# Kernel optimization log

Measured on AMD Instinct MI355X. Metric: run time of the kernel, lower is better.

The kernel has to match this reference:

```python
import jax, jax.numpy as jnp
import numpy as np

TOPK = 2


def setup_inputs() -> dict:
    key = jax.random.key(0)
    k1, k2, k3, k4, k5 = jax.random.split(key, 5)
    D, H, E = 1024, 1408, 8
    hidden_states = jax.random.normal(k1, (2, 1024, D), dtype=jnp.float32)
    gate_w = jax.random.normal(k2, (E, D), dtype=jnp.float32) * 0.02
    w1g = jax.random.normal(k3, (E, D, H), dtype=jnp.float32) * 0.02
    w1u = jax.random.normal(k4, (E, D, H), dtype=jnp.float32) * 0.02
    w2 = jax.random.normal(k5, (E, H, D), dtype=jnp.float32) * 0.02
    return {"hidden_states": hidden_states, "gate_w": gate_w, "w1g": w1g, "w1u": w1u, "w2": w2}


def reference(hidden_states, gate_w, w1g, w1u, w2):
    # hidden_states: [B, S, D]; expert weights: w1g/w1u [E, D, H], w2 [E, H, D]
    B, S, D = hidden_states.shape
    E = gate_w.shape[0]
    x = hidden_states.reshape(-1, D)  # [T, D]
    T = x.shape[0]

    # --- MoEGate: softmax scores, top-k routing (no topk renorm) ---
    logits = x @ gate_w.T                      # [T, E]
    scores = jax.nn.softmax(logits, axis=-1)   # [T, E]
    topk_w, topk_idx = jax.lax.top_k(scores, TOPK)  # [T, K]

    # Per-token combine coefficient for each expert: coeff[t, e] = sum_k w[t,k] * (idx[t,k]==e)
    coeff = jnp.zeros((T, E), dtype=x.dtype).at[jnp.arange(T)[:, None], topk_idx].add(topk_w)

    # --- Grouped expert MLP (swiglu): identical math to permute + grouped GEMM + unpermute ---
    g = jnp.einsum('td,edh->teh', x, w1g)      # [T, E, H]
    u = jnp.einsum('td,edh->teh', x, w1u)      # [T, E, H]
    h = jax.nn.silu(g) * u                     # [T, E, H]
    y = jnp.einsum('teh,te,ehd->td', h, coeff, w2)  # [T, D]
    return y.reshape(B, S, D)
```

## Files before the change

kernel.cpp:

```cpp
#include <hip/hip_runtime.h>

#define TOK 2048
#define DDIM 1024
#define HDIM 1408
#define ENUM 8
#define NSLOT (2 * TOK)
#define UP_NB 22
#define UP_KS 32
#define DN_NB 16
#define DN_KS 44

typedef unsigned int uint;
typedef unsigned short ushort;

using bf16x8 = __attribute__((ext_vector_type(8))) __bf16;
using f32x4  = __attribute__((ext_vector_type(4))) float;

__device__ __forceinline__ float silu_f(float g) {
    return g / (1.0f + __expf(-g));
}

__device__ __forceinline__ ushort cvt_bf16(float f) {
    uint u = __float_as_uint(f);
    u += 0x7FFFu + ((u >> 16) & 1u);
    return (ushort)(u >> 16);
}

__device__ __forceinline__ void gl2lds16(const void* g, void* l) {
    __builtin_amdgcn_global_load_lds(
        (const __attribute__((address_space(1))) uint*)g,
        (__attribute__((address_space(3))) uint*)l, 16, 0, 0);
}

__global__ __launch_bounds__(64) void gate_kernel(
    const float* __restrict__ x, const float* __restrict__ gw,
    int* __restrict__ counts, int* __restrict__ toks,
    float* __restrict__ wslot, ushort* __restrict__ xb)
{
    const int t = blockIdx.x;
    const int lane = threadIdx.x;
    const float* xr = x + (size_t)t * DDIM;
    ushort* xbr = xb + (size_t)t * DDIM;
    float xv[16];
#pragma unroll
    for (int i = 0; i < 16; ++i) xv[i] = xr[lane + 64 * i];
#pragma unroll
    for (int i = 0; i < 16; ++i) xbr[lane + 64 * i] = cvt_bf16(xv[i]);
    float logit[ENUM];
#pragma unroll
    for (int e = 0; e < ENUM; ++e) {
        const float* gr = gw + (size_t)e * DDIM;
        float acc = 0.f;
#pragma unroll
        for (int i = 0; i < 16; ++i) acc += xv[i] * gr[lane + 64 * i];
#pragma unroll
        for (int s = 32; s > 0; s >>= 1) acc += __shfl_xor(acc, s, 64);
        logit[e] = acc;
    }
    if (lane == 0) {
        float mx = logit[0];
#pragma unroll
        for (int e = 1; e < ENUM; ++e) mx = fmaxf(mx, logit[e]);
        float p[ENUM]; float se = 0.f;
#pragma unroll
        for (int e = 0; e < ENUM; ++e) { p[e] = __expf(logit[e] - mx); se += p[e]; }
        float inv = 1.0f / se;
#pragma unroll
        for (int e = 0; e < ENUM; ++e) p[e] *= inv;
        int i0 = 0;
#pragma unroll
        for (int e = 1; e < ENUM; ++e) if (p[e] > p[i0]) i0 = e;
        int i1 = (i0 == 0) ? 1 : 0;
#pragma unroll
        for (int e = 0; e < ENUM; ++e) if (e != i0 && p[e] > p[i1]) i1 = e;
        int pos0 = atomicAdd(&counts[i0], 1);
        toks[i0 * TOK + pos0] = (t << 1);
        wslot[(t << 1)] = p[i0];
        int pos1 = atomicAdd(&counts[i1], 1);
        toks[i1 * TOK + pos1] = (t << 1) | 1;
        wslot[(t << 1) | 1] = p[i1];
    }
}

__device__ __forceinline__ void tcast64_body(
    const float* __restrict__ src, ushort* __restrict__ dst, int N, int KS, int NB,
    int e, int ks, int nb, int tid)
{
    __shared__ float Ls[32][68];
    const float* st = src + (size_t)e * ((size_t)KS * 32) * N + (size_t)(ks * 32) * N + nb * 64;
    const int n4 = (tid & 15) * 4;
#pragma unroll
    for (int r = 0; r < 2; ++r) {
        int k = (tid >> 4) + r * 16;
        float4 v = *(const float4*)(st + (size_t)k * N + n4);
        Ls[k][n4 + 0] = v.x; Ls[k][n4 + 1] = v.y; Ls[k][n4 + 2] = v.z; Ls[k][n4 + 3] = v.w;
    }
    __syncthreads();

    ushort* dt = dst + ((((size_t)e * NB + nb) * KS) + ks) * 2048;
    const int nn = tid >> 2;
    const int kk0 = (tid & 3) * 8;
    ushort o[8];
#pragma unroll
    for (int j = 0; j < 8; ++j) o[j] = cvt_bf16(Ls[kk0 + j][nn]);
    *(uint4*)(dt + nn * 32 + kk0) = *(uint4*)o;
}

__global__ __launch_bounds__(256) void tcast_w1_kernel(
    const float* __restrict__ w1g, const float* __restrict__ w1u,
    ushort* __restrict__ BgP, ushort* __restrict__ BuP)
{
    const int z = blockIdx.z;
    const float* src = (z & 8) ? w1u : w1g;
    ushort* dst = (z & 8) ? BuP : BgP;
    tcast64_body(src, dst, HDIM, UP_KS, UP_NB, z & 7, blockIdx.x, blockIdx.y, threadIdx.x);
}

__global__ __launch_bounds__(256) void tcast_w2_kernel(
    const float* __restrict__ w2, ushort* __restrict__ W2P)
{
    tcast64_body(w2, W2P, DDIM, DN_KS, DN_NB, blockIdx.z, blockIdx.x, blockIdx.y, threadIdx.x);
}

__global__ __launch_bounds__(256, 4) void up_mfma(
    const ushort* __restrict__ xb, const ushort* __restrict__ BgP,
    const ushort* __restrict__ BuP, const int* __restrict__ counts,
    const int* __restrict__ toks, ushort* __restrict__ Hbuf)
{
    const int e = blockIdx.z;
    const int cnt = counts[e];
    const int m0 = blockIdx.y * 64;
    if (m0 >= cnt) return;
    const int nb = blockIdx.x;
    const int tid = threadIdx.x;
    const int w = tid >> 6;
    const int lane = tid & 63;
    const int q = lane >> 4;
    const int l15 = lane & 15;
    const int wr = w >> 1;
    const int wc = w & 1;

    __shared__ ushort As[2][64][32];
    __shared__ ushort Bgs[2][64][32];
    __shared__ ushort Bus[2][64][32];
    __shared__ int rowslot[64];

    if (tid < 64) rowslot[tid] = (m0 + tid < cnt) ? toks[e * TOK + m0 + tid] : -1;
    __syncthreads();

    const int arow = w * 16 + (lane >> 2);
    const int aslot = rowslot[arow];
    const ushort* agp = xb + (size_t)(aslot < 0 ? 0 : (aslot >> 1)) * DDIM + (lane & 3) * 8;
    const size_t bbase = ((size_t)(e * UP_NB + nb) * UP_KS) * 2048 + w * 512 + lane * 8;
    const ushort* bgp = BgP + bbase;
    const ushort* bup = BuP + bbase;

    f32x4 accg[2][2], accu[2][2];
#pragma unroll
    for (int i = 0; i < 2; ++i)
#pragma unroll
        for (int j = 0; j < 2; ++j) { accg[i][j] = (f32x4)0.f; accu[i][j] = (f32x4)0.f; }

#define UP_PREFETCH(KSV, B)                                   \
    {                                                         \
        gl2lds16(agp + (KSV) * 32, &As[B][w * 16][0]);        \
        gl2lds16(bgp + (size_t)(KSV) * 2048, &Bgs[B][w * 16][0]); \
        gl2lds16(bup + (size_t)(KSV) * 2048, &Bus[B][w * 16][0]); \
    }

    UP_PREFETCH(0, 0);
    __syncthreads();

    for (int ks = 0; ks < UP_KS; ++ks) {
        const int cur = ks & 1;
        const int nxt = cur ^ 1;
        if (ks + 1 < UP_KS) UP_PREFETCH(ks + 1, nxt);

        bf16x8 a[2], bg[2], bu[2];
#pragma unroll
        for (int mi = 0; mi < 2; ++mi)
            a[mi] = *(const bf16x8*)&As[cur][wr * 32 + mi * 16 + l15][q * 8];
#pragma unroll
        for (int ni = 0; ni < 2; ++ni) {
            bg[ni] = *(const bf16x8*)&Bgs[cur][wc * 32 + ni * 16 + l15][q * 8];
            bu[ni] = *(const bf16x8*)&Bus[cur][wc * 32 + ni * 16 + l15][q * 8];
        }
#pragma unroll
        for (int mi = 0; mi < 2; ++mi)
#pragma unroll
            for (int ni = 0; ni < 2; ++ni) {
                accg[mi][ni] = __builtin_amdgcn_mfma_f32_16x16x32_bf16(a[mi], bg[ni], accg[mi][ni], 0, 0, 0);
                accu[mi][ni] = __builtin_amdgcn_mfma_f32_16x16x32_bf16(a[mi], bu[ni], accu[mi][ni], 0, 0, 0);
            }
        __syncthreads();
    }
#undef UP_PREFETCH

#pragma unroll
    for (int mi = 0; mi < 2; ++mi) {
#pragma unroll
        for (int r = 0; r < 4; ++r) {
            int ml = wr * 32 + mi * 16 + q * 4 + r;
            int slot = rowslot[ml];
            if (slot < 0) continue;
            ushort* hrow = Hbuf + (size_t)slot * HDIM + nb * 64 + wc * 32 + l15;
#pragma unroll
            for (int ni = 0; ni < 2; ++ni)
                hrow[ni * 16] = cvt_bf16(silu_f(accg[mi][ni][r]) * accu[mi][ni][r]);
        }
    }
}

__global__ __launch_bounds__(256, 4) void down_mfma(
    const ushort* __restrict__ Hbuf, const ushort* __restrict__ W2P,
    const int* __restrict__ counts, const int* __restrict__ toks,
    float* __restrict__ Ybuf)
{
    const int e = blockIdx.z;
    const int cnt = counts[e];
    const int m0 = blockIdx.y * 64;
    if (m0 >= cnt) return;
    const int nb = blockIdx.x;
    const int tid = threadIdx.x;
    const int w = tid >> 6;
    const int lane = tid & 63;
    const int q = lane >> 4;
    const int l15 = lane & 15;
    const int wr = w >> 1;
    const int wc = w & 1;

    __shared__ ushort As[2][64][32];
    __shared__ ushort Bs[2][64][32];
    __shared__ int rowslot[64];

    if (tid < 64) rowslot[tid] = (m0 + tid < cnt) ? toks[e * TOK + m0 + tid] : -1;
    __syncthreads();

    const int arow = w * 16 + (lane >> 2);
    const int aslot = rowslot[arow];
    const ushort* agp = Hbuf + (size_t)(aslot < 0 ? 0 : aslot) * HDIM + (lane & 3) * 8;
    const ushort* bp = W2P + ((size_t)(e * DN_NB + nb) * DN_KS) * 2048 + w * 512 + lane * 8;

    f32x4 acc[2][2];
#pragma unroll
    for (int i = 0; i < 2; ++i)
#pragma unroll
        for (int j = 0; j < 2; ++j) acc[i][j] = (f32x4)0.f;

#define DN_PREFETCH(KSV, B)                                   \
    {                                                         \
        gl2lds16(agp + (KSV) * 32, &As[B][w * 16][0]);        \
        gl2lds16(bp + (size_t)(KSV) * 2048, &Bs[B][w * 16][0]); \
    }

    DN_PREFETCH(0, 0);
    __syncthreads();

    for (int ks = 0; ks < DN_KS; ++ks) {
        const int cur = ks & 1;
        const int nxt = cur ^ 1;
        if (ks + 1 < DN_KS) DN_PREFETCH(ks + 1, nxt);

        bf16x8 a[2], b[2];
#pragma unroll
        for (int mi = 0; mi < 2; ++mi)
            a[mi] = *(const bf16x8*)&As[cur][wr * 32 + mi * 16 + l15][q * 8];
#pragma unroll
        for (int ni = 0; ni < 2; ++ni)
            b[ni] = *(const bf16x8*)&Bs[cur][wc * 32 + ni * 16 + l15][q * 8];
#pragma unroll
        for (int mi = 0; mi < 2; ++mi)
#pragma unroll
            for (int ni = 0; ni < 2; ++ni)
                acc[mi][ni] = __builtin_amdgcn_mfma_f32_16x16x32_bf16(a[mi], b[ni], acc[mi][ni], 0, 0, 0);
        __syncthreads();
    }
#undef DN_PREFETCH

#pragma unroll
    for (int mi = 0; mi < 2; ++mi) {
#pragma unroll
        for (int r = 0; r < 4; ++r) {
            int ml = wr * 32 + mi * 16 + q * 4 + r;
            int slot = rowslot[ml];
            if (slot < 0) continue;
            float* yr = Ybuf + (size_t)slot * DDIM + nb * 64 + wc * 32 + l15;
#pragma unroll
            for (int ni = 0; ni < 2; ++ni)
                yr[ni * 16] = acc[mi][ni][r];
        }
    }
}

__global__ __launch_bounds__(256) void combine_kernel(
    const float* __restrict__ Ybuf, const float* __restrict__ wslot,
    float* __restrict__ y)
{
    const int t = blockIdx.x;
    const int j = threadIdx.x * 4;
    const float w0 = wslot[2 * t];
    const float w1 = wslot[2 * t + 1];
    float4 a = *(const float4*)(Ybuf + ((size_t)2 * t) * DDIM + j);
    float4 b = *(const float4*)(Ybuf + ((size_t)2 * t + 1) * DDIM + j);
    float4 o;
    o.x = w0 * a.x + w1 * b.x;
    o.y = w0 * a.y + w1 * b.y;
    o.z = w0 * a.z + w1 * b.z;
    o.w = w0 * a.w + w1 * b.w;
    *(float4*)(y + (size_t)t * DDIM + j) = o;
}

extern "C" void kernel_launch(void* const* d_in, const int* in_sizes, int n_in,
                              void* d_out, int out_size, void* d_ws, size_t ws_size,
                              hipStream_t stream) {
    const float* x   = (const float*)d_in[0];
    const float* gw  = (const float*)d_in[1];
    const float* w1g = (const float*)d_in[2];
    const float* w1u = (const float*)d_in[3];
    const float* w2  = (const float*)d_in[4];
    float* y = (float*)d_out;
    char* ws = (char*)d_ws;

    size_t off = 0;
    int*    counts = (int*)(ws + off);   off += 256;
    int*    toks   = (int*)(ws + off);   off += (size_t)ENUM * TOK * 4;
    float*  wslot  = (float*)(ws + off); off += (size_t)NSLOT * 4;
    off = (off + 255) & ~(size_t)255;
    ushort* xb     = (ushort*)(ws + off); off += (size_t)TOK * DDIM * 2;
    size_t regA = off;
    ushort* BgP  = (ushort*)(ws + regA);
    ushort* BuP  = (ushort*)(ws + regA + (size_t)ENUM * DDIM * HDIM * 2);
    float*  Ybuf = (float*)(ws + regA);
    off = regA + (size_t)2 * ENUM * DDIM * HDIM * 2;
    ushort* W2P  = (ushort*)(ws + off);  off += (size_t)ENUM * HDIM * DDIM * 2;
    ushort* Hbuf = (ushort*)(ws + off);

    hipMemsetAsync(counts, 0, 256, stream);

    gate_kernel<<<TOK, 64, 0, stream>>>(x, gw, counts, toks, wslot, xb);

    tcast_w1_kernel<<<dim3(UP_KS, UP_NB, 16), 256, 0, stream>>>(w1g, w1u, BgP, BuP);
    tcast_w2_kernel<<<dim3(DN_KS, DN_NB, ENUM), 256, 0, stream>>>(w2, W2P);

    up_mfma<<<dim3(UP_NB, TOK / 64, ENUM), 256, 0, stream>>>(xb, BgP, BuP, counts, toks, Hbuf);
    down_mfma<<<dim3(DN_NB, TOK / 64, ENUM), 256, 0, stream>>>(Hbuf, W2P, counts, toks, Ybuf);
    combine_kernel<<<TOK, 256, 0, stream>>>(Ybuf, wslot, y);
}
```

Baseline: 316.1 us.

## Swizzle LDS tile columns in MoE GEMMs and split routing into two kernels

Applies an XOR-style rotation of the 8-element column chunks, keyed on row, to the LDS tiles of both the up and down grouped GEMMs. Global-to-LDS loads pick rotated source columns and MFMA operand reads use the matching rotated offset, aiming to cut LDS bank conflicts on the 64-byte-row tiles. Routing now writes per-token expert ids, and a single-block second kernel builds the expert token lists with shared-memory atomics. This replaces the global atomics and the counts memset, at the cost of one extra serial launch.

```diff
diff --git a/kernel.cpp b/kernel.cpp
--- a/kernel.cpp
+++ b/kernel.cpp
@@ -32,10 +32,9 @@
         (__attribute__((address_space(3))) uint*)l, 16, 0, 0);
 }
 
-__global__ __launch_bounds__(64) void gate_kernel(
+__global__ __launch_bounds__(64) void gate1_kernel(
     const float* __restrict__ x, const float* __restrict__ gw,
-    int* __restrict__ counts, int* __restrict__ toks,
-    float* __restrict__ wslot, ushort* __restrict__ xb)
+    int* __restrict__ tinfo, float* __restrict__ wslot, ushort* __restrict__ xb)
 {
     const int t = blockIdx.x;
     const int lane = threadIdx.x;
@@ -73,13 +72,29 @@
         int i1 = (i0 == 0) ? 1 : 0;
 #pragma unroll
         for (int e = 0; e < ENUM; ++e) if (e != i0 && p[e] > p[i1]) i1 = e;
-        int pos0 = atomicAdd(&counts[i0], 1);
-        toks[i0 * TOK + pos0] = (t << 1);
+        tinfo[t] = i0 | (i1 << 4);
         wslot[(t << 1)] = p[i0];
-        int pos1 = atomicAdd(&counts[i1], 1);
-        toks[i1 * TOK + pos1] = (t << 1) | 1;
         wslot[(t << 1) | 1] = p[i1];
     }
+}
+
+__global__ __launch_bounds__(256) void gate2_kernel(
+    const int* __restrict__ tinfo, int* __restrict__ counts, int* __restrict__ toks)
+{
+    __shared__ int cnt[ENUM];
+    const int tid = threadIdx.x;
+    if (tid < ENUM) cnt[tid] = 0;
+    __syncthreads();
+    for (int t = tid; t < TOK; t += 256) {
+        int info = tinfo[t];
+        int i0 = info & 15, i1 = info >> 4;
+        int p0 = atomicAdd(&cnt[i0], 1);
+        toks[i0 * TOK + p0] = (t << 1);
+        int p1 = atomicAdd(&cnt[i1], 1);
+        toks[i1 * TOK + p1] = (t << 1) | 1;
+    }
+    __syncthreads();
+    if (tid < ENUM) counts[tid] = cnt[tid];
 }
 
 __device__ __forceinline__ void tcast64_body(
@@ -148,12 +163,15 @@
     if (tid < 64) rowslot[tid] = (m0 + tid < cnt) ? toks[e * TOK + m0 + tid] : -1;
     __syncthreads();
 
-    const int arow = w * 16 + (lane >> 2);
-    const int aslot = rowslot[arow];
-    const ushort* agp = xb + (size_t)(aslot < 0 ? 0 : (aslot >> 1)) * DDIM + (lane & 3) * 8;
-    const size_t bbase = ((size_t)(e * UP_NB + nb) * UP_KS) * 2048 + w * 512 + lane * 8;
-    const ushort* bgp = BgP + bbase;
-    const ushort* bup = BuP + bbase;
+    const int srow = w * 16 + (lane >> 2);
+    const int clog = (((lane & 3) + 4 - ((srow >> 1) & 3)) & 3) * 8;
+    const int aslot = rowslot[srow];
+    const ushort* agp = xb + (size_t)(aslot < 0 ? 0 : (aslot >> 1)) * DDIM + clog;
+    const size_t tb = (size_t)(e * UP_NB + nb) * UP_KS * 2048;
+    const ushort* bgp = BgP + tb + srow * 32 + clog;
+    const ushort* bup = BuP + tb + srow * 32 + clog;
+
+    const int coff = ((q + (l15 >> 1)) & 3) * 8;
 
     f32x4 accg[2][2], accu[2][2];
 #pragma unroll
@@ -161,9 +179,9 @@
 #pragma unroll
         for (int j = 0; j < 2; ++j) { accg[i][j] = (f32x4)0.f; accu[i][j] = (f32x4)0.f; }
 
-#define UP_PREFETCH(KSV, B)                                   \
-    {                                                         \
-        gl2lds16(agp + (KSV) * 32, &As[B][w * 16][0]);        \
+#define UP_PREFETCH(KSV, B)                                       \
+    {                                                             \
+        gl2lds16(agp + (KSV) * 32, &As[B][w * 16][0]);            \
         gl2lds16(bgp + (size_t)(KSV) * 2048, &Bgs[B][w * 16][0]); \
         gl2lds16(bup + (size_t)(KSV) * 2048, &Bus[B][w * 16][0]); \
     }
@@ -179,11 +197,11 @@
         bf16x8 a[2], bg[2], bu[2];
 #pragma unroll
         for (int mi = 0; mi < 2; ++mi)
-            a[mi] = *(const bf16x8*)&As[cur][wr * 32 + mi * 16 + l15][q * 8];
+            a[mi] = *(const bf16x8*)&As[cur][wr * 32 + mi * 16 + l15][coff];
 #pragma unroll
         for (int ni = 0; ni < 2; ++ni) {
-            bg[ni] = *(const bf16x8*)&Bgs[cur][wc * 32 + ni * 16 + l15][q * 8];
-            bu[ni] = *(const bf16x8*)&Bus[cur][wc * 32 + ni * 16 + l15][q * 8];
+            bg[ni] = *(const bf16x8*)&Bgs[cur][wc * 32 + ni * 16 + l15][coff];
+            bu[ni] = *(const bf16x8*)&Bus[cur][wc * 32 + ni * 16 + l15][coff];
         }
 #pragma unroll
         for (int mi = 0; mi < 2; ++mi)
@@ -236,10 +254,13 @@
     if (tid < 64) rowslot[tid] = (m0 + tid < cnt) ? toks[e * TOK + m0 + tid] : -1;
     __syncthreads();
 
-    const int arow = w * 16 + (lane >> 2);
-    const int aslot = rowslot[arow];
-    const ushort* agp = Hbuf + (size_t)(aslot < 0 ? 0 : aslot) * HDIM + (lane & 3) * 8;
-    const ushort* bp = W2P + ((size_t)(e * DN_NB + nb) * DN_KS) * 2048 + w * 512 + lane * 8;
+    const int srow = w * 16 + (lane >> 2);
+    const int clog = (((lane & 3) + 4 - ((srow >> 1) & 3)) & 3) * 8;
+    const int aslot = rowslot[srow];
+    const ushort* agp = Hbuf + (size_t)(aslot < 0 ? 0 : aslot) * HDIM + clog;
+    const ushort* bp = W2P + (size_t)(e * DN_NB + nb) * DN_KS * 2048 + srow * 32 + clog;
+
+    const int coff = ((q + (l15 >> 1)) & 3) * 8;
 
     f32x4 acc[2][2];
 #pragma unroll
@@ -247,9 +268,9 @@
 #pragma unroll
         for (int j = 0; j < 2; ++j) acc[i][j] = (f32x4)0.f;
 
-#define DN_PREFETCH(KSV, B)                                   \
-    {                                                         \
-        gl2lds16(agp + (KSV) * 32, &As[B][w * 16][0]);        \
+#define DN_PREFETCH(KSV, B)                                     \
+    {                                                           \
+        gl2lds16(agp + (KSV) * 32, &As[B][w * 16][0]);          \
         gl2lds16(bp + (size_t)(KSV) * 2048, &Bs[B][w * 16][0]); \
     }
 
@@ -264,10 +285,10 @@
         bf16x8 a[2], b[2];
 #pragma unroll
         for (int mi = 0; mi < 2; ++mi)
-            a[mi] = *(const bf16x8*)&As[cur][wr * 32 + mi * 16 + l15][q * 8];
+            a[mi] = *(const bf16x8*)&As[cur][wr * 32 + mi * 16 + l15][coff];
 #pragma unroll
         for (int ni = 0; ni < 2; ++ni)
-            b[ni] = *(const bf16x8*)&Bs[cur][wc * 32 + ni * 16 + l15][q * 8];
+            b[ni] = *(const bf16x8*)&Bs[cur][wc * 32 + ni * 16 + l15][coff];
 #pragma unroll
         for (int mi = 0; mi < 2; ++mi)
 #pragma unroll
@@ -325,6 +346,7 @@
     int*    counts = (int*)(ws + off);   off += 256;
     int*    toks   = (int*)(ws + off);   off += (size_t)ENUM * TOK * 4;
     float*  wslot  = (float*)(ws + off); off += (size_t)NSLOT * 4;
+    int*    tinfo  = (int*)(ws + off);   off += (size_t)TOK * 4;
     off = (off + 255) & ~(size_t)255;
     ushort* xb     = (ushort*)(ws + off); off += (size_t)TOK * DDIM * 2;
     size_t regA = off;
@@ -335,9 +357,8 @@
     ushort* W2P  = (ushort*)(ws + off);  off += (size_t)ENUM * HDIM * DDIM * 2;
     ushort* Hbuf = (ushort*)(ws + off);
 
-    hipMemsetAsync(counts, 0, 256, stream);
-
-    gate_kernel<<<TOK, 64, 0, stream>>>(x, gw, counts, toks, wslot, xb);
+    gate1_kernel<<<TOK, 64, 0, stream>>>(x, gw, tinfo, wslot, xb);
+    gate2_kernel<<<1, 256, 0, stream>>>(tinfo, counts, toks);
 
     tcast_w1_kernel<<<dim3(UP_KS, UP_NB, 16), 256, 0, stream>>>(w1g, w1u, BgP, BuP);
     tcast_w2_kernel<<<dim3(DN_KS, DN_NB, ENUM), 256, 0, stream>>>(w2, W2P);
```

New measurement: 272.0 us. -13.9%, faster.
